# Kernel optimization log

Hardware: AMD Instinct MI355X
Metric: run time of the kernel (lower is better)

Reference implementation:

```python
import jax, jax.numpy as jnp
import numpy as np

N, D, H, E, K = 8192, 1024, 2048, 8, 2

def setup_inputs() -> dict:
    key = jax.random.key(0)
    ks = jax.random.split(key, 8)
    x = jax.random.normal(ks[0], (N, D), dtype=jnp.float32)
    # Expert params stacked over the expert axis (E, ...)
    W1 = jax.random.normal(ks[1], (E, D, H), dtype=jnp.float32) * (1.0 / np.sqrt(D))
    b1 = jnp.zeros((E, H), dtype=jnp.float32)
    W2 = jax.random.normal(ks[2], (E, H, D), dtype=jnp.float32) * (1.0 / np.sqrt(H))
    b2 = jnp.zeros((E, D), dtype=jnp.float32)
    # Gating linear
    Wg = jax.random.normal(ks[3], (D, E), dtype=jnp.float32) * (1.0 / np.sqrt(D))
    bg = jnp.zeros((E,), dtype=jnp.float32)
    # Externalized gating noise (torch uses randn_like(logits) * 0.1)
    noise = jax.random.normal(ks[4], (N, E), dtype=jnp.float32)
    return {"x": x, "W1": W1, "b1": b1, "W2": W2, "b2": b2, "Wg": Wg, "bg": bg, "noise": noise}


def reference(x, W1, b1, W2, b2, Wg, bg, noise):
    n = x.shape[0]
    # --- gating: noisy top-k + softmax over top-k, scattered to dense weights ---
    logits = x @ Wg + bg                                  # [N, E]
    noisy = logits + 0.1 * noise
    top_v, top_i = jax.lax.top_k(noisy, K)                # [N, K]
    w = jax.nn.softmax(top_v, axis=-1)                    # [N, K]
    rows = jnp.arange(n)[:, None]
    sparse_w = jnp.zeros_like(logits).at[rows, top_i].set(w)  # [N, E]
    # --- all experts on all tokens (faithful to the dense-stack implementation) ---
    h = jax.nn.relu(jnp.einsum('nd,edh->neh', x, W1) + b1)    # [N, E, H]
    expert_out = jnp.einsum('neh,ehd->ned', h, W2) + b2       # [N, E, D]
    # --- weighted combine ---
    return jnp.einsum('ne,ned->nd', sparse_w, expert_out)     # [N, D]
```

## Files before the change

kernel.cpp:

```cpp
#include <hip/hip_runtime.h>
#include <stdint.h>
#include <stddef.h>

#define NTOK 8192
#define DDIM 1024
#define HDIM 2048
#define NEXP 8
#define GROWS 16384

typedef __attribute__((ext_vector_type(8))) short short8;
typedef __attribute__((ext_vector_type(8))) unsigned short ushort8;
typedef __attribute__((ext_vector_type(4))) float floatx4;

#define AS1 __attribute__((address_space(1)))
#define AS3 __attribute__((address_space(3)))

#define MAXRT 136
#define MAXT1 (MAXRT * (HDIM / 128))
#define MAXT2 (MAXRT * (DDIM / 128))

constexpr size_t OFF_CNT  = 0;
constexpr size_t OFF_TB1  = 256;
constexpr size_t OFF_TB2  = OFF_TB1 + 8960;
constexpr size_t OFF_TKI  = OFF_TB2 + 4608;
constexpr size_t OFF_TKW  = OFF_TKI + (size_t)NTOK * 8;
constexpr size_t OFF_LIST = OFF_TKW + (size_t)NTOK * 8;
constexpr size_t OFF_WTS  = OFF_LIST + (size_t)NEXP * NTOK * 4;
constexpr size_t OFF_XBF  = OFF_WTS + (size_t)NEXP * NTOK * 4;
constexpr size_t OFF_AKB  = OFF_XBF + (size_t)NTOK * DDIM * 2;
constexpr size_t OFF_W1KB = OFF_AKB + (size_t)GROWS * DDIM * 2;
constexpr size_t OFF_W2KB = OFF_W1KB + (size_t)NEXP * DDIM * HDIM * 2;
constexpr size_t OFF_HKB  = OFF_W2KB + (size_t)NEXP * DDIM * HDIM * 2;

__device__ __forceinline__ unsigned short f2bf(float f) {
  union { float f; unsigned u; } v; v.f = f;
  unsigned r = v.u + 0x7FFFu + ((v.u >> 16) & 1u);
  return (unsigned short)(r >> 16);
}

__global__ __launch_bounds__(256) void gate_kernel(
    const float* __restrict__ x, const float* __restrict__ Wg,
    const float* __restrict__ bg, const float* __restrict__ noise,
    int2* __restrict__ tki, float2* __restrict__ tkw,
    unsigned short* __restrict__ xbf) {
  int lane = threadIdx.x & 63;
  int wid  = threadIdx.x >> 6;
  int token = blockIdx.x * 4 + wid;
  const float* xr = x + (size_t)token * DDIM;
  unsigned short* xo = xbf + (size_t)token * DDIM;
  double acc[NEXP];
#pragma unroll
  for (int e = 0; e < NEXP; ++e) acc[e] = 0.0;
  for (int d = lane; d < DDIM; d += 64) {
    float xv = xr[d];
    xo[d] = f2bf(xv);
    const floatx4* wp = (const floatx4*)(Wg + d * NEXP);
    floatx4 w0 = wp[0], w1 = wp[1];
#pragma unroll
    for (int j = 0; j < 4; ++j) {
      acc[j]     += (double)xv * (double)w0[j];
      acc[4 + j] += (double)xv * (double)w1[j];
    }
  }
#pragma unroll
  for (int e = 0; e < NEXP; ++e)
#pragma unroll
    for (int off = 32; off > 0; off >>= 1) acc[e] += __shfl_xor(acc[e], off);
  if (lane == 0) {
    float nv[NEXP];
#pragma unroll
    for (int e = 0; e < NEXP; ++e) {
      float lg = (float)(acc[e] + (double)bg[e]);
      nv[e] = lg + 0.1f * noise[token * NEXP + e];
    }
    int i1 = 0; float v1 = nv[0];
#pragma unroll
    for (int e = 1; e < NEXP; ++e) if (nv[e] > v1) { v1 = nv[e]; i1 = e; }
    int i2 = -1; float v2 = -3.4e38f;
#pragma unroll
    for (int e = 0; e < NEXP; ++e) if (e != i1 && nv[e] > v2) { v2 = nv[e]; i2 = e; }
    float tt  = expf(v2 - v1);
    tki[token] = make_int2(i1, i2);
    tkw[token] = make_float2(1.0f / (1.0f + tt), tt / (1.0f + tt));
  }
}

__global__ __launch_bounds__(256) void scatter_kernel(
    const int2* __restrict__ tki, const float2* __restrict__ tkw,
    int* __restrict__ counts, int* __restrict__ lists, float* __restrict__ wts) {
  int e = blockIdx.x;
  int tid = threadIdx.x;
  int lane = tid & 63, wid = tid >> 6;
  __shared__ int wave_cnt[4];
  __shared__ int run_total;
  if (tid == 0) run_total = 0;
  __syncthreads();
  for (int t0 = 0; t0 < NTOK; t0 += 256) {
    int tok = t0 + tid;
    int2 ki = tki[tok];
    float2 kw = tkw[tok];
    bool sel = (ki.x == e) || (ki.y == e);
    float w = (ki.x == e) ? kw.x : kw.y;
    unsigned long long mask = __ballot(sel);
    int pos = __popcll(mask & ((1ull << lane) - 1ull));
    if (lane == 0) wave_cnt[wid] = __popcll(mask);
    __syncthreads();
    int base = run_total;
    for (int i = 0; i < wid; ++i) base += wave_cnt[i];
    if (sel) {
      lists[e * NTOK + base + pos] = tok;
      wts[e * NTOK + base + pos] = w;
    }
    __syncthreads();
    if (tid == 0) run_total += wave_cnt[0] + wave_cnt[1] + wave_cnt[2] + wave_cnt[3];
    __syncthreads();
  }
  if (tid == 0) counts[e] = run_total;
}

__global__ __launch_bounds__(256) void gather_a_kernel(
    const unsigned short* __restrict__ xbf, const int* __restrict__ counts,
    const int* __restrict__ lists, unsigned short* __restrict__ akb) {
  int kt   = blockIdx.y;
  int grow = blockIdx.x * 256 + threadIdx.x;
  int c[8];
#pragma unroll
  for (int i = 0; i < 8; ++i) c[i] = counts[i];
  int e = 0, off = 0;
#pragma unroll
  for (int i = 0; i < 8; ++i)
    if (e == i && grow >= off + c[i]) { off += c[i]; e = i + 1; }
  int tok = lists[e * NTOK + (grow - off)];
  const ushort8* s = (const ushort8*)(xbf + (size_t)tok * DDIM + kt * 32);
  ushort8* d = (ushort8*)(akb + (size_t)kt * GROWS * 32 + (size_t)grow * 32);
  d[0] = s[0]; d[1] = s[1]; d[2] = s[2]; d[3] = s[3];
}

__global__ __launch_bounds__(256) void build_tiles_kernel(
    const int* __restrict__ counts, int* __restrict__ tb1, int* __restrict__ tb2) {
  int tid = threadIdx.x;
  int ct[8], cum[9];
  cum[0] = 0;
#pragma unroll
  for (int e = 0; e < 8; ++e) { ct[e] = (counts[e] + 127) >> 7; cum[e + 1] = cum[e] + ct[e]; }
  int nt = cum[8];
  constexpr int NBY1 = HDIM / 128, NBY2 = DDIM / 128;
  if (tid == 0) { tb1[0] = nt * NBY1; tb2[0] = nt * NBY2; }
  for (int idx = tid; idx < nt * NBY1; idx += 256) {
    int e = 0;
    while (idx >= cum[e + 1] * NBY1) ++e;
    int r = idx - cum[e] * NBY1;
    int by = r / ct[e], bx = r - by * ct[e];
    tb1[1 + idx] = (e << 16) | (bx << 8) | by;
  }
  for (int idx = tid; idx < nt * NBY2; idx += 256) {
    int e = 0;
    while (idx >= cum[e + 1] * NBY2) ++e;
    int r = idx - cum[e] * NBY2;
    int by = r / ct[e], bx = r - by * ct[e];
    tb2[1 + idx] = (e << 16) | (bx << 8) | by;
  }
}

__global__ __launch_bounds__(256) void transpose_cvt_kernel(
    const float* __restrict__ W, unsigned short* __restrict__ WT, int R, int C) {
  __shared__ float tile[64][65];
  int e = blockIdx.z;
  const float* Win = W + (size_t)e * R * C;
  unsigned short* Wout = WT + (size_t)e * R * C;
  int c0 = blockIdx.x * 64, r0 = blockIdx.y * 64;
  int tx = threadIdx.x & 63, ty = threadIdx.x >> 6;
#pragma unroll
  for (int i = ty; i < 64; i += 4)
    tile[i][tx] = Win[(size_t)(r0 + i) * C + c0 + tx];
  __syncthreads();
  int cc = threadIdx.x >> 2, seg = (threadIdx.x & 3) * 16;
  ushort8 o0, o1;
#pragma unroll
  for (int j = 0; j < 8; ++j) o0[j] = f2bf(tile[seg + j][cc]);
#pragma unroll
  for (int j = 0; j < 8; ++j) o1[j] = f2bf(tile[seg + 8 + j][cc]);
  int koff = r0 + seg;
  unsigned short* outp = Wout + (size_t)(koff >> 5) * C * 32
                              + (size_t)(c0 + cc) * 32 + (koff & 31);
  *(ushort8*)(outp) = o0;
  *(ushort8*)(outp + 8) = o1;
}

template <int KDIM, int NDIM, bool IS_G1>
__global__ __launch_bounds__(512, 4) void moe_gemm_kernel(
    const unsigned short* __restrict__ Akb,
    const unsigned short* __restrict__ Bkb,
    const float* __restrict__ bias,
    const int* __restrict__ counts, const int* __restrict__ lists,
    const float* __restrict__ wts, const int* __restrict__ tbl,
    unsigned short* __restrict__ Hkb,
    float* __restrict__ Out) {
  __shared__ __align__(16) char smem[32768];
  constexpr int NT = KDIM / 32;
  constexpr size_t A_KT = (size_t)GROWS * 32;
  constexpr size_t B_KT = (size_t)NDIM * 32;

  int ntiles = tbl[0];
  int bid = blockIdx.x;
  if (bid >= ntiles) return;
  int q = ntiles >> 3, rr = ntiles & 7;
  int xcd = bid & 7, within = bid >> 3;
  int widx = (xcd < rr ? xcd * (q + 1) : rr * (q + 1) + (xcd - rr) * q) + within;
  int desc = tbl[1 + widx];
  int e  = desc >> 16;
  int bx = (desc >> 8) & 0xff;
  int by = desc & 0xff;

  int Me, off_e = 0;
  {
    int c[8];
#pragma unroll
    for (int i = 0; i < 8; ++i) c[i] = counts[i];
    Me = c[e];
#pragma unroll
    for (int i = 0; i < 8; ++i) if (i < e) off_e += c[i];
  }

  int tid = threadIdx.x;
  int lane = tid & 63, wid = tid >> 6;
  int wr = wid >> 2, wc = wid & 3;
  int r16 = lane & 15, g4 = lane >> 4;

  int r0 = tid >> 2;
  int ch = ((tid & 3) ^ ((r0 >> 1) & 3)) * 8;
  const unsigned short *sA, *sB;
  {
    int lr = bx * 128 + r0;
    int g = off_e + (lr < Me ? lr : 0);
    sA = Akb + (size_t)g * 32 + ch;
    sB = Bkb + (size_t)e * KDIM * NDIM + (size_t)(by * 128 + r0) * 32 + ch;
  }

  auto stage = [&](int t) {
    int buf = t & 1;
    char* da = smem + buf * 8192 + tid * 16;
    char* db = smem + 16384 + buf * 8192 + tid * 16;
    __builtin_amdgcn_global_load_lds((const AS1 void*)(sA + (size_t)t * A_KT), (AS3 void*)da, 16, 0, 0);
    __builtin_amdgcn_global_load_lds((const AS1 void*)(sB + (size_t)t * B_KT), (AS3 void*)db, 16, 0, 0);
  };

  int aoff[4], boff[2];
#pragma unroll
  for (int m = 0; m < 4; ++m) {
    int rowa = wr * 64 + m * 16 + r16;
    aoff[m] = rowa * 64 + ((g4 ^ ((rowa >> 1) & 3)) * 16);
  }
#pragma unroll
  for (int n = 0; n < 2; ++n) {
    int rowb = wc * 32 + n * 16 + r16;
    boff[n] = 16384 + rowb * 64 + ((g4 ^ ((rowb >> 1) & 3)) * 16);
  }

  floatx4 acc[4][2];
#pragma unroll
  for (int m = 0; m < 4; ++m)
#pragma unroll
    for (int n = 0; n < 2; ++n) acc[m][n] = (floatx4){0.f, 0.f, 0.f, 0.f};

  stage(0);
  stage(1);

  for (int t = 0; t < NT; ++t) {
    if (t + 1 < NT) { asm volatile("s_waitcnt vmcnt(2)" ::: "memory"); }
    else            { asm volatile("s_waitcnt vmcnt(0)" ::: "memory"); }
    __builtin_amdgcn_s_barrier();
    __builtin_amdgcn_sched_barrier(0);
    const char* pa = smem + (t & 1) * 8192;
    const char* pb = smem + (t & 1) * 8192;
    short8 a[4], b[2];
#pragma unroll
    for (int m = 0; m < 4; ++m) a[m] = *(const short8*)(pa + aoff[m]);
#pragma unroll
    for (int n = 0; n < 2; ++n) b[n] = *(const short8*)(pb + boff[n]);
#pragma unroll
    for (int m = 0; m < 4; ++m)
#pragma unroll
      for (int n = 0; n < 2; ++n)
        acc[m][n] = __builtin_amdgcn_mfma_f32_16x16x32_bf16(a[m], b[n], acc[m][n], 0, 0, 0);
    __builtin_amdgcn_s_barrier();
    __builtin_amdgcn_sched_barrier(0);
    if (t + 2 < NT) stage(t + 2);
  }

  if constexpr (IS_G1) {
#pragma unroll
    for (int m = 0; m < 4; ++m) {
#pragma unroll
      for (int i = 0; i < 4; ++i) {
        int lrow = bx * 128 + wr * 64 + m * 16 + g4 * 4 + i;
        if (lrow < Me) {
          size_t grow = (size_t)(off_e + lrow);
#pragma unroll
          for (int n = 0; n < 2; ++n) {
            int col = by * 128 + wc * 32 + n * 16 + r16;
            float v = acc[m][n][i] + bias[e * NDIM + col];
            Hkb[(size_t)(col >> 5) * A_KT + grow * 32 + (col & 31)] = f2bf(fmaxf(v, 0.f));
          }
        }
      }
    }
  } else {
#pragma unroll
    for (int m = 0; m < 4; ++m) {
#pragma unroll
      for (int i = 0; i < 4; ++i) {
        int lrow = bx * 128 + wr * 64 + m * 16 + g4 * 4 + i;
        if (lrow < Me) {
          int tok = lists[e * NTOK + lrow];
          float w = wts[e * NTOK + lrow];
          float* orow = Out + (size_t)tok * NDIM + by * 128;
#pragma unroll
          for (int n = 0; n < 2; ++n) {
            int col = wc * 32 + n * 16 + r16;
            float v = acc[m][n][i] + bias[e * NDIM + by * 128 + col];
            atomicAdd(orow + col, w * v);
          }
        }
      }
    }
  }
}

extern "C" void kernel_launch(void* const* d_in, const int* in_sizes, int n_in,
                              void* d_out, int out_size, void* d_ws, size_t ws_size,
                              hipStream_t stream) {
  (void)in_sizes; (void)n_in; (void)ws_size;
  const float* x     = (const float*)d_in[0];
  const float* W1    = (const float*)d_in[1];
  const float* b1    = (const float*)d_in[2];
  const float* W2    = (const float*)d_in[3];
  const float* b2    = (const float*)d_in[4];
  const float* Wg    = (const float*)d_in[5];
  const float* bg    = (const float*)d_in[6];
  const float* noise = (const float*)d_in[7];
  float* out = (float*)d_out;

  char* ws = (char*)d_ws;
  int*            counts = (int*)(ws + OFF_CNT);
  int*            tb1    = (int*)(ws + OFF_TB1);
  int*            tb2    = (int*)(ws + OFF_TB2);
  int2*           tki    = (int2*)(ws + OFF_TKI);
  float2*         tkw    = (float2*)(ws + OFF_TKW);
  int*            lists  = (int*)(ws + OFF_LIST);
  float*          wts    = (float*)(ws + OFF_WTS);
  unsigned short* xbf    = (unsigned short*)(ws + OFF_XBF);
  unsigned short* akb    = (unsigned short*)(ws + OFF_AKB);
  unsigned short* w1kb   = (unsigned short*)(ws + OFF_W1KB);
  unsigned short* w2kb   = (unsigned short*)(ws + OFF_W2KB);
  unsigned short* hkb    = (unsigned short*)(ws + OFF_HKB);

  hipMemsetAsync(d_out, 0, (size_t)out_size * sizeof(float), stream);
  hipMemsetAsync(counts, 0, 256, stream);

  gate_kernel<<<NTOK / 4, 256, 0, stream>>>(x, Wg, bg, noise, tki, tkw, xbf);
  scatter_kernel<<<NEXP, 256, 0, stream>>>(tki, tkw, counts, lists, wts);
  build_tiles_kernel<<<1, 256, 0, stream>>>(counts, tb1, tb2);
  gather_a_kernel<<<dim3(GROWS / 256, DDIM / 32), 256, 0, stream>>>(xbf, counts, lists, akb);
  transpose_cvt_kernel<<<dim3(HDIM / 64, DDIM / 64, NEXP), 256, 0, stream>>>(W1, w1kb, DDIM, HDIM);
  transpose_cvt_kernel<<<dim3(DDIM / 64, HDIM / 64, NEXP), 256, 0, stream>>>(W2, w2kb, HDIM, DDIM);

  moe_gemm_kernel<DDIM, HDIM, true>
      <<<MAXT1, 512, 0, stream>>>(akb, w1kb, b1, counts, lists, wts, tb1, hkb, nullptr);
  moe_gemm_kernel<HDIM, DDIM, false>
      <<<MAXT2, 512, 0, stream>>>(hkb, w2kb, b2, counts, lists, wts, tb2, nullptr, out);
}
```

Before: 341.9 us.

## Use 1024-thread blocks for MoE GEMM, splitting A/B staging across halves

Doubles the GEMM workgroup to 16 waves, so each wave computes a 32x32 sub-tile instead of 64x32 of the same 128x128 block tile. The first 512 threads stage the A tile and the second 512 stage the B tile, one global-to-LDS load each per k-step, so the vmcnt wait drops from 2 to 1. The aim is more waves in flight to hide memory latency, but each wave now does half as many MFMAs between barriers. That lowers per-wave data reuse and raises barrier cost relative to compute.

```diff
diff --git a/kernel.cpp b/kernel.cpp
--- a/kernel.cpp
+++ b/kernel.cpp
@@ -188,7 +188,7 @@
 }
 
 template <int KDIM, int NDIM, bool IS_G1>
-__global__ __launch_bounds__(512, 4) void moe_gemm_kernel(
+__global__ __launch_bounds__(1024, 8) void moe_gemm_kernel(
     const unsigned short* __restrict__ Akb,
     const unsigned short* __restrict__ Bkb,
     const float* __restrict__ bias,
@@ -227,39 +227,41 @@
   int wr = wid >> 2, wc = wid & 3;
   int r16 = lane & 15, g4 = lane >> 4;
 
-  int r0 = tid >> 2;
-  int ch = ((tid & 3) ^ ((r0 >> 1) & 3)) * 8;
-  const unsigned short *sA, *sB;
-  {
+  int t2 = tid & 511;
+  int r0 = t2 >> 2;
+  int ch = ((t2 & 3) ^ ((r0 >> 1) & 3)) * 8;
+  const unsigned short* sp;
+  size_t step;
+  if (tid < 512) {
     int lr = bx * 128 + r0;
     int g = off_e + (lr < Me ? lr : 0);
-    sA = Akb + (size_t)g * 32 + ch;
-    sB = Bkb + (size_t)e * KDIM * NDIM + (size_t)(by * 128 + r0) * 32 + ch;
+    sp = Akb + (size_t)g * 32 + ch;
+    step = A_KT;
+  } else {
+    sp = Bkb + (size_t)e * KDIM * NDIM + (size_t)(by * 128 + r0) * 32 + ch;
+    step = B_KT;
   }
 
   auto stage = [&](int t) {
-    int buf = t & 1;
-    char* da = smem + buf * 8192 + tid * 16;
-    char* db = smem + 16384 + buf * 8192 + tid * 16;
-    __builtin_amdgcn_global_load_lds((const AS1 void*)(sA + (size_t)t * A_KT), (AS3 void*)da, 16, 0, 0);
-    __builtin_amdgcn_global_load_lds((const AS1 void*)(sB + (size_t)t * B_KT), (AS3 void*)db, 16, 0, 0);
+    char* d = smem + (t & 1) * 16384 + tid * 16;
+    __builtin_amdgcn_global_load_lds((const AS1 void*)(sp + (size_t)t * step), (AS3 void*)d, 16, 0, 0);
   };
 
-  int aoff[4], boff[2];
-#pragma unroll
-  for (int m = 0; m < 4; ++m) {
-    int rowa = wr * 64 + m * 16 + r16;
+  int aoff[2], boff[2];
+#pragma unroll
+  for (int m = 0; m < 2; ++m) {
+    int rowa = wr * 32 + m * 16 + r16;
     aoff[m] = rowa * 64 + ((g4 ^ ((rowa >> 1) & 3)) * 16);
   }
 #pragma unroll
   for (int n = 0; n < 2; ++n) {
     int rowb = wc * 32 + n * 16 + r16;
-    boff[n] = 16384 + rowb * 64 + ((g4 ^ ((rowb >> 1) & 3)) * 16);
-  }
-
-  floatx4 acc[4][2];
-#pragma unroll
-  for (int m = 0; m < 4; ++m)
+    boff[n] = 8192 + rowb * 64 + ((g4 ^ ((rowb >> 1) & 3)) * 16);
+  }
+
+  floatx4 acc[2][2];
+#pragma unroll
+  for (int m = 0; m < 2; ++m)
 #pragma unroll
     for (int n = 0; n < 2; ++n) acc[m][n] = (floatx4){0.f, 0.f, 0.f, 0.f};
 
@@ -267,19 +269,18 @@
   stage(1);
 
   for (int t = 0; t < NT; ++t) {
-    if (t + 1 < NT) { asm volatile("s_waitcnt vmcnt(2)" ::: "memory"); }
+    if (t + 1 < NT) { asm volatile("s_waitcnt vmcnt(1)" ::: "memory"); }
     else            { asm volatile("s_waitcnt vmcnt(0)" ::: "memory"); }
     __builtin_amdgcn_s_barrier();
     __builtin_amdgcn_sched_barrier(0);
-    const char* pa = smem + (t & 1) * 8192;
-    const char* pb = smem + (t & 1) * 8192;
-    short8 a[4], b[2];
-#pragma unroll
-    for (int m = 0; m < 4; ++m) a[m] = *(const short8*)(pa + aoff[m]);
-#pragma unroll
-    for (int n = 0; n < 2; ++n) b[n] = *(const short8*)(pb + boff[n]);
-#pragma unroll
-    for (int m = 0; m < 4; ++m)
+    const char* p = smem + (t & 1) * 16384;
+    short8 a[2], b[2];
+#pragma unroll
+    for (int m = 0; m < 2; ++m) a[m] = *(const short8*)(p + aoff[m]);
+#pragma unroll
+    for (int n = 0; n < 2; ++n) b[n] = *(const short8*)(p + boff[n]);
+#pragma unroll
+    for (int m = 0; m < 2; ++m)
 #pragma unroll
       for (int n = 0; n < 2; ++n)
         acc[m][n] = __builtin_amdgcn_mfma_f32_16x16x32_bf16(a[m], b[n], acc[m][n], 0, 0, 0);
@@ -290,10 +291,10 @@
 
   if constexpr (IS_G1) {
 #pragma unroll
-    for (int m = 0; m < 4; ++m) {
+    for (int m = 0; m < 2; ++m) {
 #pragma unroll
       for (int i = 0; i < 4; ++i) {
-        int lrow = bx * 128 + wr * 64 + m * 16 + g4 * 4 + i;
+        int lrow = bx * 128 + wr * 32 + m * 16 + g4 * 4 + i;
         if (lrow < Me) {
           size_t grow = (size_t)(off_e + lrow);
 #pragma unroll
@@ -307,10 +308,10 @@
     }
   } else {
 #pragma unroll
-    for (int m = 0; m < 4; ++m) {
+    for (int m = 0; m < 2; ++m) {
 #pragma unroll
       for (int i = 0; i < 4; ++i) {
-        int lrow = bx * 128 + wr * 64 + m * 16 + g4 * 4 + i;
+        int lrow = bx * 128 + wr * 32 + m * 16 + g4 * 4 + i;
         if (lrow < Me) {
           int tok = lists[e * NTOK + lrow];
           float w = wts[e * NTOK + lrow];
@@ -366,7 +367,7 @@
   transpose_cvt_kernel<<<dim3(DDIM / 64, HDIM / 64, NEXP), 256, 0, stream>>>(W2, w2kb, HDIM, DDIM);
 
   moe_gemm_kernel<DDIM, HDIM, true>
-      <<<MAXT1, 512, 0, stream>>>(akb, w1kb, b1, counts, lists, wts, tb1, hkb, nullptr);
+      <<<MAXT1, 1024, 0, stream>>>(akb, w1kb, b1, counts, lists, wts, tb1, hkb, nullptr);
   moe_gemm_kernel<HDIM, DDIM, false>
-      <<<MAXT2, 512, 0, stream>>>(hkb, w2kb, b2, counts, lists, wts, tb2, nullptr, out);
-}
+      <<<MAXT2, 1024, 0, stream>>>(hkb, w2kb, b2, counts, lists, wts, tb2, nullptr, out);
+}
```

Result: slower. 360.4 us (+5.4%).
